# Kernel optimization log

Hardware: AMD Instinct MI355X
Metric: run time of the kernel (lower is better)

## Reference

```python
import jax, jax.numpy as jnp
import numpy as np

K = 16        # num_p
SIGMA = 1.0
B, NA, NB, C = 2, 16384, 8192, 128
Z, Y, X = 64, 256, 256  # spatial_shape


def _unique_coords(rng, n):
    lin = rng.choice(Z * Y * X, size=n, replace=False)
    z = lin // (Y * X)
    y = (lin // X) % Y
    x = lin % X
    return np.stack([z, y, x], axis=-1).astype(np.float32)


def setup_inputs() -> dict:
    key = jax.random.key(0)
    k1, = jax.random.split(key, 1)
    rng = np.random.default_rng(0)
    # teacher voxel coords unique per batch -> bev_out_3d dedup is identity
    tpos = np.stack([_unique_coords(rng, NA) for _ in range(B)])          # [B, NA, 3]
    spos = np.stack([_unique_coords(rng, NB) for _ in range(B)])          # [B, NB, 3]
    tfeat = jax.random.normal(k1, (B, NA, C), dtype=jnp.float32)
    return {
        "teacher_features": tfeat,
        "teacher_positions": jnp.asarray(tpos),
        "student_positions": jnp.asarray(spos),
    }


def _knn_agg(feats, pa, pb):
    # feats: [NA, C], pa: [NA, 3] teacher coords, pb: [NB, 3] student coords
    # squared euclidean distances (same top-k ordering as cdist p=2)
    sq = (jnp.sum(pb * pb, -1, keepdims=True)
          - 2.0 * pb @ pa.T
          + jnp.sum(pa * pa, -1)[None, :])                                # [NB, NA]
    neg_sq_k, idx = jax.lax.top_k(-sq, K)                                 # smallest-k
    knn_sq = jnp.maximum(-neg_sq_k, 0.0)                                  # [NB, K] = knn_dist**2
    w = jnp.exp(-knn_sq / (2.0 * SIGMA ** 2))
    w = w / jnp.sum(w, axis=1, keepdims=True)
    knn_feats = feats[idx]                                                # [NB, K, C]
    return jnp.einsum('nkc,nk->nc', knn_feats, w)                         # [NB, C]


def reference(teacher_features, teacher_positions, student_positions):
    # per-batch knn_aggregation, batches have equal sizes -> vmap
    return jax.vmap(_knn_agg)(teacher_features, teacher_positions, student_positions)
```

## Files before the change

### kernel.cpp

```cpp
#include <hip/hip_runtime.h>
#include <math.h>
#include <stdint.h>

#define K_NN   16
#define BATCH  2
#define NA_    16384
#define NB_    8192
#define CH     128
#define CZ     4
#define CY     16
#define CX     16
#define NCELL  (CZ*CY*CX)
#define CSH    4
#define PADKEY 0xFFF00000u

#define OFF_META   65536
#define OFF_SORTED 98304

__device__ __forceinline__ int cell_of(float p0, float p1, float p2) {
    const int cz = ((int)p0) >> CSH;
    const int cy = ((int)p1) >> CSH;
    const int cx = ((int)p2) >> CSH;
    return (cz * CY + cy) * CX + cx;
}


__global__ __launch_bounds__(256) void count_hist(const float* __restrict__ tpos,
                                                  int* __restrict__ partial) {
    __shared__ int h[NCELL];
    const int blk = blockIdx.x;
    const int t = threadIdx.x;
#pragma unroll
    for (int j = 0; j < NCELL / 256; ++j) h[t + j * 256] = 0;
    __syncthreads();
    const int base = blk * 2048;
#pragma unroll
    for (int i = 0; i < 8; ++i) {
        const float* p = tpos + (size_t)(base + i * 256 + t) * 3;
        atomicAdd(&h[cell_of(p[0], p[1], p[2])], 1);
    }
    __syncthreads();
#pragma unroll
    for (int j = 0; j < NCELL / 256; ++j) {
        const int c = t + j * 256;
        partial[blk * NCELL + c] = h[c];
    }
}


__global__ __launch_bounds__(256) void scan_scatter(const float* __restrict__ tpos,
                                                    const int* __restrict__ partial,
                                                    int2* __restrict__ meta,
                                                    uint2* __restrict__ sorted) {
    __shared__ int sCur[NCELL];
    __shared__ int wp[4];

    const int h = blockIdx.x;
    const int b = h >> 3, hl = h & 7;
    const int t = threadIdx.x;
    const int lane = t & 63, w = t >> 6;

    int tot0 = 0, tot1 = 0, tot2 = 0, tot3 = 0;
    int pre0 = 0, pre1 = 0, pre2 = 0, pre3 = 0;
#pragma unroll
    for (int k = 0; k < 8; ++k) {
        const int4 v = *(const int4*)(partial + (b * 8 + k) * NCELL + t * 4);
        tot0 += v.x; tot1 += v.y; tot2 += v.z; tot3 += v.w;
        if (k < hl) { pre0 += v.x; pre1 += v.y; pre2 += v.z; pre3 += v.w; }
    }
    const int tsum = tot0 + tot1 + tot2 + tot3;
    int x = tsum;
#pragma unroll
    for (int off = 1; off < 64; off <<= 1) {
        int u = __shfl_up(x, off);
        if (lane >= off) x += u;
    }
    if (lane == 63) wp[w] = x;
    __syncthreads();
    if (t == 0) {
        int r = 0;
#pragma unroll
        for (int k = 0; k < 4; ++k) { const int v = wp[k]; wp[k] = r; r += v; }
    }
    __syncthreads();
    int e = x - tsum + wp[w];
    const int c0 = t * 4;
    if (hl == 0) {
        meta[b * NCELL + c0 + 0] = make_int2(e, tot0);
        meta[b * NCELL + c0 + 1] = make_int2(e + tot0, tot1);
        meta[b * NCELL + c0 + 2] = make_int2(e + tot0 + tot1, tot2);
        meta[b * NCELL + c0 + 3] = make_int2(e + tot0 + tot1 + tot2, tot3);
    }
    sCur[c0 + 0] = e + pre0;
    sCur[c0 + 1] = e + tot0 + pre1;
    sCur[c0 + 2] = e + tot0 + tot1 + pre2;
    sCur[c0 + 3] = e + tot0 + tot1 + tot2 + pre3;
    __syncthreads();

    const float* tb = tpos + (size_t)(b * NA_ + hl * 2048) * 3;
#pragma unroll
    for (int i = 0; i < 8; ++i) {
        const int pi = i * 256 + t;
        const float* p = tb + (size_t)pi * 3;
        const int pz = (int)p[0], py = (int)p[1], px = (int)p[2];
        const int cell = ((pz >> CSH) * CY + (py >> CSH)) * CX + (px >> CSH);
        const int pos = atomicAdd(&sCur[cell], 1);
        const uint32_t pk = ((uint32_t)pz << 16) | ((uint32_t)py << 8) | (uint32_t)px;
        sorted[(size_t)b * NA_ + pos] = make_uint2(pk, (uint32_t)(hl * 2048 + pi));
    }
}


template<int NS>
__device__ __forceinline__ void merge_extract(uint32_t (&k)[NS], uint32_t (&sel)[K_NN]) {
    uint32_t m = k[0];
#pragma unroll
    for (int j = 1; j < NS; ++j) m = min(m, k[j]);
#pragma unroll
    for (int r = 0; r < K_NN; ++r) {
        uint32_t v = m;
#pragma unroll
        for (int off = 32; off > 0; off >>= 1)
            v = min(v, (uint32_t)__shfl_xor((int)v, off));
        sel[r] = (uint32_t)__builtin_amdgcn_readfirstlane((int)v);
        if (m == v) {
#pragma unroll
            for (int j = 0; j < NS; ++j) k[j] = (k[j] == v) ? 0xFFFFFFFFu : k[j];
            m = k[0];
#pragma unroll
            for (int j = 1; j < NS; ++j) m = min(m, k[j]);
        }
    }
}

__device__ __forceinline__ uint32_t key_of(uint2 p, int sz, int sy, int sx) {
    const int pz = (int)(p.x >> 16);
    const int py = (int)((p.x >> 8) & 255u);
    const int px = (int)(p.x & 255u);
    const int dz = sz - pz, dy = sy - py, dx = sx - px;
    const uint32_t d2 = (uint32_t)(dz * dz + dy * dy + dx * dx);
    return (d2 << 14) | p.y;
}


__device__ __noinline__ void ring_fallback(int lane, int sz, int sy, int sx,
                                           int scz, int scy, int scx, int rcov,
                                           const int2* __restrict__ mb,
                                           const uint2* __restrict__ sb,
                                           uint32_t* selLds) {
    uint32_t sel[K_NN];
#pragma unroll
    for (int j = 0; j < K_NN; ++j) sel[j] = 0xFFFFFFFFu;

    for (int r = 1;; ++r) {
        uint32_t kl[K_NN];
#pragma unroll
        for (int j = 0; j < K_NN; ++j) kl[j] = PADKEY + 16 + j;
        if (r > 1) {
            uint32_t seed = 0xFFFFFFFFu;
#pragma unroll
            for (int j = 0; j < K_NN; ++j) if (lane == j) seed = sel[j];
            kl[0] = seed;
        }
        uint32_t curmax = kl[0];
#pragma unroll
        for (int j = 1; j < K_NN; ++j) curmax = max(curmax, kl[j]);

        for (int dz = -r; dz <= r; ++dz) {
            const int cz = scz + dz; if ((unsigned)cz >= CZ) continue;
            for (int dy = -r; dy <= r; ++dy) {
                const int cy = scy + dy; if ((unsigned)cy >= CY) continue;
                const int rowb = (cz * CY + cy) * CX;
                const bool fullrow = (r == 1) || (max(abs(dz), abs(dy)) == r);
                int xl[2], xh[2];
                if (fullrow) {
                    xl[0] = max(scx - r, 0); xh[0] = min(scx + r, CX - 1);
                    xl[1] = 1; xh[1] = 0;
                } else {
                    xl[0] = scx - r; xh[0] = scx - r;
                    xl[1] = scx + r; xh[1] = scx + r;
                    if (xl[0] < 0)      { xl[0] = 1; xh[0] = 0; }
                    if (xh[1] > CX - 1) { xl[1] = 1; xh[1] = 0; }
                }
#pragma unroll
                for (int q = 0; q < 2; ++q) {
                    if (xl[q] > xh[q]) continue;
                    const int2 mlo = mb[rowb + xl[q]];
                    const int2 mhi = mb[rowb + xh[q]];
                    const int st = mlo.x, ln = mhi.x + mhi.y - st;
                    for (int o = 0; o < ln; o += 64) {
                        const int j2 = o + lane;
                        const bool act = j2 < ln;
                        const uint2 p = sb[st + (act ? j2 : 0)];
                        uint32_t kv = key_of(p, sz, sy, sx);
                        kv = act ? kv : 0xFFFFFFFFu;
                        if (kv < curmax) {
#pragma unroll
                            for (int j = 0; j < K_NN; ++j)
                                kl[j] = (kl[j] == curmax) ? kv : kl[j];
                            curmax = kl[0];
#pragma unroll
                            for (int j = 1; j < K_NN; ++j) curmax = max(curmax, kl[j]);
                        }
                    }
                }
            }
        }
        merge_extract<K_NN>(kl, sel);
        const uint32_t d16 = sel[K_NN - 1] >> 14;
        if (d16 <= (uint32_t)(256 * r * r) || r >= rcov) break;
    }

    if (lane == 0) {
#pragma unroll
        for (int j = 0; j < K_NN; ++j) selLds[j] = sel[j];
    }
}


__global__ __launch_bounds__(256) void knn_cells_kernel(
    const float* __restrict__ tfeat,
    const float* __restrict__ spos,
    const int2*  __restrict__ meta,
    const uint2* __restrict__ sorted,
    float* __restrict__ out)
{
    __shared__ uint32_t sSel[4][16];

    const int tid  = threadIdx.x;
    const int lane = tid & 63;
    const int wave = tid >> 6;

    const int bpb = NB_ / 4;
    const int b = blockIdx.x / bpb;
    const int n = (blockIdx.x % bpb) * 4 + wave;

    const float* sp = spos + ((size_t)b * NB_ + n) * 3;
    const int sz = (int)sp[0], sy = (int)sp[1], sx = (int)sp[2];
    const int scz = __builtin_amdgcn_readfirstlane(sz >> CSH);
    const int scy = __builtin_amdgcn_readfirstlane(sy >> CSH);
    const int scx = __builtin_amdgcn_readfirstlane(sx >> CSH);

    int rcov = max(max(scx, CX - 1 - scx), max(scy, CY - 1 - scy));
    rcov = max(rcov, max(scz, CZ - 1 - scz));

    const int2*  mb = meta   + (size_t)b * NCELL;
    const uint2* sb = sorted + (size_t)b * NA_;

    int rstart[9], rlen[9];
    const int cxlo = max(scx - 1, 0), cxhi = min(scx + 1, CX - 1);
    int nov = 0; bool fast = true;
#pragma unroll
    for (int kk = 0; kk < 9; ++kk) {
        const int cz = scz + kk / 3 - 1, cy = scy + kk % 3 - 1;
        int st = 0, ln = 0;
        if ((unsigned)cz < CZ && (unsigned)cy < CY) {
            const int rowb = (cz * CY + cy) * CX;
            const int2 mlo = mb[rowb + cxlo];
            const int2 mhi = mb[rowb + cxhi];
            st = mlo.x; ln = mhi.x + mhi.y - mlo.x;
        }
        rstart[kk] = st; rlen[kk] = ln;
        if (ln > 64) ++nov;
        if (ln > 128) fast = false;
    }
    if (nov > 3) fast = false;

    int nselF = K_NN;
    bool done = false;

    if (fast) {
        uint32_t key[12];
#pragma unroll
        for (int j = 0; j < 12; ++j) key[j] = PADKEY + j;
        int oc = 9;
#pragma unroll
        for (int kk = 0; kk < 9; ++kk) {
            if (rlen[kk] > 0) {
                const bool act = lane < rlen[kk];
                const uint2 p = sb[rstart[kk] + (act ? lane : 0)];
                const uint32_t kv = key_of(p, sz, sy, sx);
                key[kk] = act ? kv : key[kk];
            }
            if (rlen[kk] > 64) {
                const int j2 = 64 + lane;
                const bool act = j2 < rlen[kk];
                const uint2 p = sb[rstart[kk] + (act ? j2 : 0)];
                const uint32_t kv = key_of(p, sz, sy, sx);
                if (oc == 9)       key[9]  = act ? kv : key[9];
                else if (oc == 10) key[10] = act ? kv : key[10];
                else               key[11] = act ? kv : key[11];
                ++oc;
            }
        }

        uint32_t kmin = key[0];
#pragma unroll
        for (int j = 1; j < 12; ++j) kmin = min(kmin, key[j]);
#pragma unroll
        for (int off = 32; off > 0; off >>= 1)
            kmin = min(kmin, (uint32_t)__shfl_xor((int)kmin, off));
        kmin = (uint32_t)__builtin_amdgcn_readfirstlane((int)kmin);
        const uint32_t dmin2 = kmin >> 14;

        if (dmin2 <= 264u) {
            const uint32_t keyT = (dmin2 + 25u) << 14;
            int nsel = 0;
#pragma unroll
            for (int j = 0; j < 12; ++j) {
                const bool pred = key[j] < keyT;
                const unsigned long long m = __ballot(pred);
                const int offp = __builtin_amdgcn_mbcnt_hi(
                    (uint32_t)(m >> 32), __builtin_amdgcn_mbcnt_lo((uint32_t)m, 0));
                const int dst = nsel + offp;
                if (pred && dst < K_NN) sSel[wave][dst] = key[j];
                nsel += (int)__builtin_popcountll(m);
            }
            if (nsel <= K_NN) {
                nselF = nsel;
                done = true;
            }
        }
    }

    if (!done)
        ring_fallback(lane, sz, sy, sx, scz, scy, scx, rcov, mb, sb, &sSel[wave][0]);
    __threadfence_block();

    const uint4 sA = *(const uint4*)&sSel[wave][0];
    const uint4 sB = *(const uint4*)&sSel[wave][4];
    const uint4 sC = *(const uint4*)&sSel[wave][8];
    const uint4 sD = *(const uint4*)&sSel[wave][12];
    uint32_t sel[K_NN];
    sel[0]  = (uint32_t)__builtin_amdgcn_readfirstlane((int)sA.x);
    sel[1]  = (uint32_t)__builtin_amdgcn_readfirstlane((int)sA.y);
    sel[2]  = (uint32_t)__builtin_amdgcn_readfirstlane((int)sA.z);
    sel[3]  = (uint32_t)__builtin_amdgcn_readfirstlane((int)sA.w);
    sel[4]  = (uint32_t)__builtin_amdgcn_readfirstlane((int)sB.x);
    sel[5]  = (uint32_t)__builtin_amdgcn_readfirstlane((int)sB.y);
    sel[6]  = (uint32_t)__builtin_amdgcn_readfirstlane((int)sB.z);
    sel[7]  = (uint32_t)__builtin_amdgcn_readfirstlane((int)sB.w);
    sel[8]  = (uint32_t)__builtin_amdgcn_readfirstlane((int)sC.x);
    sel[9]  = (uint32_t)__builtin_amdgcn_readfirstlane((int)sC.y);
    sel[10] = (uint32_t)__builtin_amdgcn_readfirstlane((int)sC.z);
    sel[11] = (uint32_t)__builtin_amdgcn_readfirstlane((int)sC.w);
    sel[12] = (uint32_t)__builtin_amdgcn_readfirstlane((int)sD.x);
    sel[13] = (uint32_t)__builtin_amdgcn_readfirstlane((int)sD.y);
    sel[14] = (uint32_t)__builtin_amdgcn_readfirstlane((int)sD.z);
    sel[15] = (uint32_t)__builtin_amdgcn_readfirstlane((int)sD.w);

    float w[K_NN];
    float wsum = 0.f;
#pragma unroll
    for (int j = 0; j < K_NN; ++j) w[j] = 0.f;
#pragma unroll
    for (int j = 0; j < 4; ++j) {
        if (j < nselF) { w[j] = __expf(-0.5f * (float)(sel[j] >> 14)); wsum += w[j]; }
    }
    if (nselF > 4) {
#pragma unroll
        for (int j = 4; j < 8; ++j) {
            if (j < nselF) { w[j] = __expf(-0.5f * (float)(sel[j] >> 14)); wsum += w[j]; }
        }
    }
    if (nselF > 8) {
#pragma unroll
        for (int j = 8; j < 12; ++j) {
            if (j < nselF) { w[j] = __expf(-0.5f * (float)(sel[j] >> 14)); wsum += w[j]; }
        }
    }
    if (nselF > 12) {
#pragma unroll
        for (int j = 12; j < 16; ++j) {
            if (j < nselF) { w[j] = __expf(-0.5f * (float)(sel[j] >> 14)); wsum += w[j]; }
        }
    }
    const float inv = 1.0f / wsum;

    const float* fb = tfeat + (size_t)b * NA_ * CH;
    float2 acc = make_float2(0.f, 0.f);
#pragma unroll
    for (int j = 0; j < 4; ++j) {
        if (j < nselF) {
            const float2 v = ((const float2*)(fb + (size_t)(sel[j] & 16383u) * CH))[lane];
            const float ww = w[j] * inv;
            acc.x += ww * v.x; acc.y += ww * v.y;
        }
    }
    if (nselF > 4) {
#pragma unroll
        for (int j = 4; j < 8; ++j) {
            if (j < nselF) {
                const float2 v = ((const float2*)(fb + (size_t)(sel[j] & 16383u) * CH))[lane];
                const float ww = w[j] * inv;
                acc.x += ww * v.x; acc.y += ww * v.y;
            }
        }
    }
    if (nselF > 8) {
#pragma unroll
        for (int j = 8; j < 12; ++j) {
            if (j < nselF) {
                const float2 v = ((const float2*)(fb + (size_t)(sel[j] & 16383u) * CH))[lane];
                const float ww = w[j] * inv;
                acc.x += ww * v.x; acc.y += ww * v.y;
            }
        }
    }
    if (nselF > 12) {
#pragma unroll
        for (int j = 12; j < 16; ++j) {
            if (j < nselF) {
                const float2 v = ((const float2*)(fb + (size_t)(sel[j] & 16383u) * CH))[lane];
                const float ww = w[j] * inv;
                acc.x += ww * v.x; acc.y += ww * v.y;
            }
        }
    }

    float2* o = (float2*)(out + ((size_t)b * NB_ + n) * CH);
    o[lane] = acc;
}


extern "C" void kernel_launch(void* const* d_in, const int* in_sizes, int n_in,
                              void* d_out, int out_size, void* d_ws, size_t ws_size,
                              hipStream_t stream) {
    const float* tfeat = (const float*)d_in[0];
    const float* tpos  = (const float*)d_in[1];
    const float* spos  = (const float*)d_in[2];
    float* out = (float*)d_out;

    char* ws = (char*)d_ws;
    int*   partial = (int*)(ws);
    int2*  meta    = (int2*)(ws + OFF_META);
    uint2* sorted  = (uint2*)(ws + OFF_SORTED);

    count_hist<<<16, 256, 0, stream>>>(tpos, partial);
    scan_scatter<<<16, 256, 0, stream>>>(tpos, partial, meta, sorted);
    knn_cells_kernel<<<BATCH * (NB_ / 4), 256, 0, stream>>>(tfeat, spos, meta, sorted, out);
}
```

Baseline: 38.13 us.

## Fuse histogram and scan-scatter into one grid-build kernel with redundant counting

Replaces the separate count_hist and scan_scatter kernels with one build_one kernel. Each of the 16 blocks recomputes the full per-batch cell histogram in shared memory, reading positions with float4 loads, and snapshots the prefix counts when it reaches its own chunk. This removes one kernel launch and the global partial-histogram round trip. In exchange each block reads 8x more position data and performs 8x more shared atomics. Within a cell, point order now depends on atomic order and differs from before, which could affect tie ordering downstream.

```diff
diff --git a/kernel.cpp b/kernel.cpp
--- a/kernel.cpp
+++ b/kernel.cpp
@@ -17,42 +17,12 @@
 #define OFF_META   65536
 #define OFF_SORTED 98304
 
-__device__ __forceinline__ int cell_of(float p0, float p1, float p2) {
-    const int cz = ((int)p0) >> CSH;
-    const int cy = ((int)p1) >> CSH;
-    const int cx = ((int)p2) >> CSH;
-    return (cz * CY + cy) * CX + cx;
-}
-
-
-__global__ __launch_bounds__(256) void count_hist(const float* __restrict__ tpos,
-                                                  int* __restrict__ partial) {
-    __shared__ int h[NCELL];
-    const int blk = blockIdx.x;
-    const int t = threadIdx.x;
-#pragma unroll
-    for (int j = 0; j < NCELL / 256; ++j) h[t + j * 256] = 0;
-    __syncthreads();
-    const int base = blk * 2048;
-#pragma unroll
-    for (int i = 0; i < 8; ++i) {
-        const float* p = tpos + (size_t)(base + i * 256 + t) * 3;
-        atomicAdd(&h[cell_of(p[0], p[1], p[2])], 1);
-    }
-    __syncthreads();
-#pragma unroll
-    for (int j = 0; j < NCELL / 256; ++j) {
-        const int c = t + j * 256;
-        partial[blk * NCELL + c] = h[c];
-    }
-}
-
-
-__global__ __launch_bounds__(256) void scan_scatter(const float* __restrict__ tpos,
-                                                    const int* __restrict__ partial,
-                                                    int2* __restrict__ meta,
-                                                    uint2* __restrict__ sorted) {
-    __shared__ int sCur[NCELL];
+
+__global__ __launch_bounds__(256) void build_one(const float* __restrict__ tpos,
+                                                 int2* __restrict__ meta,
+                                                 uint2* __restrict__ sorted) {
+    __shared__ int sH[NCELL];
+    __shared__ int sP[NCELL];
     __shared__ int wp[4];
 
     const int h = blockIdx.x;
@@ -60,14 +30,48 @@
     const int t = threadIdx.x;
     const int lane = t & 63, w = t >> 6;
 
-    int tot0 = 0, tot1 = 0, tot2 = 0, tot3 = 0;
-    int pre0 = 0, pre1 = 0, pre2 = 0, pre3 = 0;
-#pragma unroll
+#pragma unroll
+    for (int j = 0; j < 4; ++j) sH[t + j * 256] = 0;
+    __syncthreads();
+
+    const float* tb = tpos + (size_t)b * NA_ * 3;
+    uint32_t mypk[8];
+    int      mycell[8];
+
     for (int k = 0; k < 8; ++k) {
-        const int4 v = *(const int4*)(partial + (b * 8 + k) * NCELL + t * 4);
-        tot0 += v.x; tot1 += v.y; tot2 += v.z; tot3 += v.w;
-        if (k < hl) { pre0 += v.x; pre1 += v.y; pre2 += v.z; pre3 += v.w; }
-    }
+        if (k == hl) {
+            __syncthreads();
+#pragma unroll
+            for (int j = 0; j < 4; ++j) sP[t + j * 256] = sH[t + j * 256];
+            __syncthreads();
+        }
+        const float4* f4 = (const float4*)(tb + (size_t)(k * 2048 + t * 8) * 3);
+        const float4 f0 = f4[0], f1 = f4[1], f2 = f4[2];
+        const float4 f3 = f4[3], f4v = f4[4], f5 = f4[5];
+#pragma unroll
+        for (int i = 0; i < 8; ++i) {
+            float pzf, pyf, pxf;
+            if      (i == 0) { pzf = f0.x;  pyf = f0.y;  pxf = f0.z; }
+            else if (i == 1) { pzf = f0.w;  pyf = f1.x;  pxf = f1.y; }
+            else if (i == 2) { pzf = f1.z;  pyf = f1.w;  pxf = f2.x; }
+            else if (i == 3) { pzf = f2.y;  pyf = f2.z;  pxf = f2.w; }
+            else if (i == 4) { pzf = f3.x;  pyf = f3.y;  pxf = f3.z; }
+            else if (i == 5) { pzf = f3.w;  pyf = f4v.x; pxf = f4v.y; }
+            else if (i == 6) { pzf = f4v.z; pyf = f4v.w; pxf = f5.x; }
+            else             { pzf = f5.y;  pyf = f5.z;  pxf = f5.w; }
+            const int pz = (int)pzf, py = (int)pyf, px = (int)pxf;
+            const int cell = ((pz >> CSH) * CY + (py >> CSH)) * CX + (px >> CSH);
+            atomicAdd(&sH[cell], 1);
+            if (k == hl) {
+                mypk[i] = ((uint32_t)pz << 16) | ((uint32_t)py << 8) | (uint32_t)px;
+                mycell[i] = cell;
+            }
+        }
+    }
+    __syncthreads();
+
+    const int c0 = t * 4;
+    const int tot0 = sH[c0], tot1 = sH[c0 + 1], tot2 = sH[c0 + 2], tot3 = sH[c0 + 3];
     const int tsum = tot0 + tot1 + tot2 + tot3;
     int x = tsum;
 #pragma unroll
@@ -83,30 +87,26 @@
         for (int k = 0; k < 4; ++k) { const int v = wp[k]; wp[k] = r; r += v; }
     }
     __syncthreads();
-    int e = x - tsum + wp[w];
-    const int c0 = t * 4;
+    const int e = x - tsum + wp[w];
     if (hl == 0) {
         meta[b * NCELL + c0 + 0] = make_int2(e, tot0);
         meta[b * NCELL + c0 + 1] = make_int2(e + tot0, tot1);
         meta[b * NCELL + c0 + 2] = make_int2(e + tot0 + tot1, tot2);
         meta[b * NCELL + c0 + 3] = make_int2(e + tot0 + tot1 + tot2, tot3);
     }
-    sCur[c0 + 0] = e + pre0;
-    sCur[c0 + 1] = e + tot0 + pre1;
-    sCur[c0 + 2] = e + tot0 + tot1 + pre2;
-    sCur[c0 + 3] = e + tot0 + tot1 + tot2 + pre3;
-    __syncthreads();
-
-    const float* tb = tpos + (size_t)(b * NA_ + hl * 2048) * 3;
+    const int p0 = sP[c0], p1 = sP[c0 + 1], p2 = sP[c0 + 2], p3 = sP[c0 + 3];
+    __syncthreads();
+    sH[c0 + 0] = e + p0;
+    sH[c0 + 1] = e + tot0 + p1;
+    sH[c0 + 2] = e + tot0 + tot1 + p2;
+    sH[c0 + 3] = e + tot0 + tot1 + tot2 + p3;
+    __syncthreads();
+
 #pragma unroll
     for (int i = 0; i < 8; ++i) {
-        const int pi = i * 256 + t;
-        const float* p = tb + (size_t)pi * 3;
-        const int pz = (int)p[0], py = (int)p[1], px = (int)p[2];
-        const int cell = ((pz >> CSH) * CY + (py >> CSH)) * CX + (px >> CSH);
-        const int pos = atomicAdd(&sCur[cell], 1);
-        const uint32_t pk = ((uint32_t)pz << 16) | ((uint32_t)py << 8) | (uint32_t)px;
-        sorted[(size_t)b * NA_ + pos] = make_uint2(pk, (uint32_t)(hl * 2048 + pi));
+        const int pos = atomicAdd(&sH[mycell[i]], 1);
+        sorted[(size_t)b * NA_ + pos] =
+            make_uint2(mypk[i], (uint32_t)(hl * 2048 + t * 8 + i));
     }
 }
 
@@ -432,11 +432,9 @@
     float* out = (float*)d_out;
 
     char* ws = (char*)d_ws;
-    int*   partial = (int*)(ws);
-    int2*  meta    = (int2*)(ws + OFF_META);
-    uint2* sorted  = (uint2*)(ws + OFF_SORTED);
-
-    count_hist<<<16, 256, 0, stream>>>(tpos, partial);
-    scan_scatter<<<16, 256, 0, stream>>>(tpos, partial, meta, sorted);
+    int2*  meta   = (int2*)(ws + OFF_META);
+    uint2* sorted = (uint2*)(ws + OFF_SORTED);
+
+    build_one<<<16, 256, 0, stream>>>(tpos, meta, sorted);
     knn_cells_kernel<<<BATCH * (NB_ / 4), 256, 0, stream>>>(tfeat, spos, meta, sorted, out);
 }
```

After: 37.35 us. -2.0%, faster.
